# Performance work log

Measured on AMD Instinct MI355X. Metric: run time of the kernel, lower is better.

Reference implementation:

```python
import jax, jax.numpy as jnp
import numpy as np

B, H, W, D, C = 1, 32, 32, 32, 256
WS = (8, 8, 8)
SS = (4, 4, 4)
NH = 8
HD = C // NH
N = WS[0] * WS[1] * WS[2]
NW = (H // WS[0]) * (W // WS[1]) * (D // WS[2])


def _rel_pos_index():
    coords = np.stack(np.meshgrid(np.arange(WS[0]), np.arange(WS[1]), np.arange(WS[2]), indexing='ij'))
    cf = coords.reshape(3, -1)
    rc = (cf[:, :, None] - cf[:, None, :]).transpose(1, 2, 0).astype(np.int64)
    rc[:, :, 0] += WS[0] - 1
    rc[:, :, 1] += WS[1] - 1
    rc[:, :, 2] += WS[2] - 1
    rc[:, :, 0] *= (2 * WS[2] - 1) * (2 * WS[1] - 1)
    rc[:, :, 1] *= (2 * WS[2] - 1)
    return rc.sum(-1).reshape(-1)  # [N*N]


def _attn_mask():
    m = np.zeros((H, W, D), np.float32)
    cnt = 0

    def sl(ws, ss):
        return ((0, -ws), (-ws, -ss), (-ss, None))

    for hs in sl(WS[0], SS[0]):
        for ws_ in sl(WS[1], SS[1]):
            for ds in sl(WS[2], SS[2]):
                m[hs[0]:hs[1], ws_[0]:ws_[1], ds[0]:ds[1]] = cnt
                cnt += 1
    m = m.reshape(H // WS[0], WS[0], W // WS[1], WS[1], D // WS[2], WS[2])
    m = m.transpose(0, 2, 4, 1, 3, 5).reshape(NW, N)
    diff = m[:, None, :] - m[:, :, None]  # [NW, N, N]
    return np.where(diff != 0, -100.0, 0.0).astype(np.float32)


REL_IDX = jnp.asarray(_rel_pos_index())
ATTN_MASK = jnp.asarray(_attn_mask())  # [NW, N, N]


def setup_inputs() -> dict:
    key = jax.random.key(0)
    ks = jax.random.split(key, 4)
    return {
        'x': jax.random.normal(ks[0], (B, H, W, D, C), jnp.float32),
        'qkv_weight': jax.random.normal(ks[1], (3 * C, C), jnp.float32) * 0.02,
        'qkv_bias': jnp.zeros((3 * C,), jnp.float32),
        'proj_weight': jax.random.normal(ks[2], (C, C), jnp.float32) * 0.02,
        'proj_bias': jnp.zeros((C,), jnp.float32),
        'rpb_table': jax.random.normal(ks[3], ((2 * WS[0] - 1) * (2 * WS[1] - 1) * (2 * WS[2] - 1), NH), jnp.float32) * 0.02,
    }


def reference(x, qkv_weight, qkv_bias, proj_weight, proj_bias, rpb_table):
    # cyclic shift
    xs = jnp.roll(x, (-SS[0], -SS[1], -SS[2]), axis=(1, 2, 3))
    # window partition -> [B*NW, N, C]
    xw = xs.reshape(B, H // WS[0], WS[0], W // WS[1], WS[1], D // WS[2], WS[2], C)
    xw = xw.transpose(0, 1, 3, 5, 2, 4, 6, 7).reshape(B * NW, N, C)
    # qkv projection
    qkv = xw @ qkv_weight.T + qkv_bias
    qkv = qkv.reshape(B * NW, N, 3, NH, HD).transpose(2, 0, 3, 1, 4)  # [3, B*NW, NH, N, HD]
    q, k, v = qkv[0] * (HD ** -0.5), qkv[1], qkv[2]
    # relative position bias [NH, N, N]
    bias = rpb_table[REL_IDX].reshape(N, N, NH).transpose(2, 0, 1)
    attn = jnp.einsum('whnd,whmd->whnm', q, k) + bias[None]
    # shift mask per window
    attn = attn.reshape(B, NW, NH, N, N) + ATTN_MASK[None, :, None]
    attn = jax.nn.softmax(attn.reshape(B * NW, NH, N, N), axis=-1)
    out = jnp.einsum('whnm,whmd->whnd', attn, v)
    out = out.transpose(0, 2, 1, 3).reshape(B * NW, N, C)
    out = out @ proj_weight.T + proj_bias
    # un-window -> [B, H, W, D, C]
    out = out.reshape(B, H // WS[0], W // WS[1], D // WS[2], WS[0], WS[1], WS[2], C)
    out = out.transpose(0, 1, 4, 2, 5, 3, 6, 7).reshape(B, H, W, D, C)
    # reverse cyclic shift
    return jnp.roll(out, (SS[0], SS[1], SS[2]), axis=(1, 2, 3))
```

## Files before the change

### kernel.cpp

```cpp
#include <hip/hip_runtime.h>

typedef __attribute__((ext_vector_type(8))) short short8;
typedef __attribute__((ext_vector_type(4))) short s4v;
typedef __attribute__((ext_vector_type(2))) uint uint2v;
typedef __attribute__((ext_vector_type(4))) float floatx4;

#define CCH   256
#define QSCALE 0.17677669529663687f
#define LOG2E  1.4426950408889634f

__device__ __forceinline__ unsigned short f2bf(float f) {
    unsigned u = __float_as_uint(f);
    u = u + 0x7fffu + ((u >> 16) & 1u);
    return (unsigned short)(u >> 16);
}

__device__ __forceinline__ uint pk2bf(float a, float b) {
    uint ua = __float_as_uint(a) + 0x8000u;
    uint ub = __float_as_uint(b) + 0x8000u;
    return __builtin_amdgcn_perm(ub, ua, 0x07060302u);
}

__device__ __forceinline__ void gl_lds16(const void* g, void* l) {
    __builtin_amdgcn_global_load_lds((const __attribute__((address_space(1))) void*)g,
                                     (__attribute__((address_space(3))) void*)l, 16, 0, 0);
}

__device__ __forceinline__ int spatial_off(int token) {
    int w = token >> 9, n = token & 511;
    int wh = w >> 4, ww = (w >> 2) & 3, wd = w & 3;
    int h1 = n >> 6, w1 = (n >> 3) & 7, d1 = n & 7;
    int gh = (wh * 8 + h1 + 4) & 31;
    int gw = (ww * 8 + w1 + 4) & 31;
    int gd = (wd * 8 + d1 + 4) & 31;
    return ((gh * 32 + gw) * 32 + gd) * CCH;
}

__global__ __launch_bounds__(256) void xconv(const float* __restrict__ x,
                                             ushort* __restrict__ Xw) {
    int tid = blockIdx.x * 256 + threadIdx.x;
    int token = tid >> 5, c8 = (tid & 31) * 8;
    const float* src = x + spatial_off(token) + c8;
    float4 a = *(const float4*)src;
    float4 b = *(const float4*)(src + 4);
    uint2v lo, hi;
    lo[0] = pk2bf(a.x, a.y);
    lo[1] = pk2bf(a.z, a.w);
    hi[0] = pk2bf(b.x, b.y);
    hi[1] = pk2bf(b.z, b.w);
    uint2v* dst = (uint2v*)(Xw + (size_t)token * 256 + c8);
    dst[0] = lo;
    dst[1] = hi;
}

__global__ __launch_bounds__(256) void wconv(const float* __restrict__ Wq,
                                             const float* __restrict__ Wp,
                                             ushort* __restrict__ Wqb,
                                             ushort* __restrict__ Wpb) {
    int tid = blockIdx.x * 256 + threadIdx.x;
    if (tid < 196608) {
        float s = (tid < 65536) ? (QSCALE * LOG2E) : 1.0f;
        Wqb[tid] = f2bf(Wq[tid] * s);
    } else {
        int i = tid - 196608;
        Wpb[i] = f2bf(Wp[i]);
    }
}

__global__ __launch_bounds__(256) void pair_prep(const float* __restrict__ rpb,
                                                 uint* __restrict__ Up) {
    int tid = blockIdx.x * 256 + threadIdx.x;
    if (tid >= 27000) return;
    int head = tid / 3375, idx = tid - head * 3375;
    uint lo = f2bf(rpb[idx * 8 + head] * LOG2E);
    uint hi = f2bf(rpb[(idx > 0 ? idx - 1 : 0) * 8 + head] * LOG2E);
    Up[tid] = lo | (hi << 16);
}

__global__ __launch_bounds__(256) void gemm_qkv(
    const ushort* __restrict__ A,
    const ushort* __restrict__ Bw,
    const float* __restrict__ bq,
    ushort* __restrict__ Q, ushort* __restrict__ K, ushort* __restrict__ Vf) {
    __shared__ short As[128 * 64];
    __shared__ short Bs[128 * 64];
    const int t = threadIdx.x;
    const int wv = t >> 6, lane = t & 63, quad = lane >> 4, col = lane & 15;
    const int m0 = blockIdx.y * 128, n0 = blockIdx.x * 128;
    const int wm = (wv & 1) * 64, wn = (wv >> 1) * 64;

    floatx4 zf = {0.f, 0.f, 0.f, 0.f};
    floatx4 acc[4][4];
#pragma unroll
    for (int i = 0; i < 4; ++i)
#pragma unroll
        for (int j = 0; j < 4; ++j) acc[i][j] = zf;

    for (int kk = 0; kk < 256; kk += 64) {
        __syncthreads();
#pragma unroll
        for (int i = 0; i < 4; ++i) {
            int s = i * 256 + t;
            int row = s >> 3, qs = s & 7;
            int qg = qs ^ (row & 7);
            gl_lds16(A + (size_t)(m0 + row) * 256 + kk + qg * 8,
                     As + (i * 256 + wv * 64) * 8);
        }
#pragma unroll
        for (int i = 0; i < 4; ++i) {
            int s = i * 256 + t;
            int row = s >> 3, qs = s & 7;
            int qg = qs ^ (row & 7);
            gl_lds16(Bw + (size_t)(n0 + row) * 256 + kk + qg * 8,
                     Bs + (i * 256 + wv * 64) * 8);
        }
        __syncthreads();
#pragma unroll
        for (int h = 0; h < 2; ++h) {
            short8 af[4], bf[4];
#pragma unroll
            for (int mi = 0; mi < 4; ++mi) {
                int row = wm + mi * 16 + col;
                af[mi] = *(const short8*)(As + (row * 8 + ((h * 4 + quad) ^ (row & 7))) * 8);
            }
#pragma unroll
            for (int ni = 0; ni < 4; ++ni) {
                int row = wn + ni * 16 + col;
                bf[ni] = *(const short8*)(Bs + (row * 8 + ((h * 4 + quad) ^ (row & 7))) * 8);
            }
#pragma unroll
            for (int mi = 0; mi < 4; ++mi)
#pragma unroll
                for (int ni = 0; ni < 4; ++ni)
                    acc[mi][ni] = __builtin_amdgcn_mfma_f32_16x16x32_bf16(af[mi], bf[ni], acc[mi][ni], 0, 0, 0);
        }
    }

#pragma unroll
    for (int ni = 0; ni < 4; ++ni) {
        int j = n0 + wn + ni * 16 + col;
        int three = j >> 8, head = (j >> 5) & 7, hd = j & 31;
        float bias = bq[j] * ((j < 256) ? (QSCALE * LOG2E) : 1.0f);
        if (three == 2) {
            int h = hd >> 4, colv = hd & 15;
#pragma unroll
            for (int mi = 0; mi < 4; ++mi) {
                int mb = m0 + wm + mi * 16 + quad * 4;
                int w = mb >> 9, n = mb & 511;
                size_t off = ((size_t)((w * 8 + head) * 64 + (n >> 4) * 2 + h) << 8)
                           + ((((n >> 2) & 3) * 16 + colv) << 2);
                uint2v pv;
                pv[0] = pk2bf(acc[mi][ni][0] + bias, acc[mi][ni][1] + bias);
                pv[1] = pk2bf(acc[mi][ni][2] + bias, acc[mi][ni][3] + bias);
                *(uint2v*)(Vf + off) = pv;
            }
        } else {
            ushort* dst = (three == 0) ? Q : K;
#pragma unroll
            for (int mi = 0; mi < 4; ++mi) {
#pragma unroll
                for (int r = 0; r < 4; ++r) {
                    int m = m0 + wm + mi * 16 + quad * 4 + r;
                    int w = m >> 9, n = m & 511;
                    dst[((size_t)(w * 8 + head) * 512 + n) * 32 + hd] = f2bf(acc[mi][ni][r] + bias);
                }
            }
        }
    }
}

__global__ __launch_bounds__(256) void gemm_proj(
    const ushort* __restrict__ A,
    const ushort* __restrict__ Bw,
    const float* __restrict__ bp,
    float* __restrict__ out) {
    __shared__ short As[128 * 64];
    __shared__ short Bs[128 * 64];
    const int t = threadIdx.x;
    const int wv = t >> 6, lane = t & 63, quad = lane >> 4, col = lane & 15;
    const int m0 = blockIdx.y * 128, n0 = blockIdx.x * 128;
    const int wm = (wv & 1) * 64, wn = (wv >> 1) * 64;

    floatx4 zf = {0.f, 0.f, 0.f, 0.f};
    floatx4 acc[4][4];
#pragma unroll
    for (int i = 0; i < 4; ++i)
#pragma unroll
        for (int j = 0; j < 4; ++j) acc[i][j] = zf;

    for (int kk = 0; kk < 256; kk += 64) {
        __syncthreads();
#pragma unroll
        for (int i = 0; i < 4; ++i) {
            int s = i * 256 + t;
            int row = s >> 3, qs = s & 7;
            int qg = qs ^ (row & 7);
            gl_lds16(A + (size_t)(m0 + row) * 256 + kk + qg * 8,
                     As + (i * 256 + wv * 64) * 8);
        }
#pragma unroll
        for (int i = 0; i < 4; ++i) {
            int s = i * 256 + t;
            int row = s >> 3, qs = s & 7;
            int qg = qs ^ (row & 7);
            gl_lds16(Bw + (size_t)(n0 + row) * 256 + kk + qg * 8,
                     Bs + (i * 256 + wv * 64) * 8);
        }
        __syncthreads();
#pragma unroll
        for (int h = 0; h < 2; ++h) {
            short8 af[4], bf[4];
#pragma unroll
            for (int mi = 0; mi < 4; ++mi) {
                int row = wm + mi * 16 + col;
                af[mi] = *(const short8*)(As + (row * 8 + ((h * 4 + quad) ^ (row & 7))) * 8);
            }
#pragma unroll
            for (int ni = 0; ni < 4; ++ni) {
                int row = wn + ni * 16 + col;
                bf[ni] = *(const short8*)(Bs + (row * 8 + ((h * 4 + quad) ^ (row & 7))) * 8);
            }
#pragma unroll
            for (int mi = 0; mi < 4; ++mi)
#pragma unroll
                for (int ni = 0; ni < 4; ++ni)
                    acc[mi][ni] = __builtin_amdgcn_mfma_f32_16x16x32_bf16(af[mi], bf[ni], acc[mi][ni], 0, 0, 0);
        }
    }

#pragma unroll
    for (int ni = 0; ni < 4; ++ni) {
        int j = n0 + wn + ni * 16 + col;
        float bias = bp[j];
#pragma unroll
        for (int mi = 0; mi < 4; ++mi) {
#pragma unroll
            for (int r = 0; r < 4; ++r) {
                int m = m0 + wm + mi * 16 + quad * 4 + r;
                out[spatial_off(m) + j] = acc[mi][ni][r] + bias;
            }
        }
    }
}

__global__ __launch_bounds__(256, 2) void attn_kernel(
    const ushort* __restrict__ Q, const ushort* __restrict__ K,
    const ushort* __restrict__ Vf, const uint* __restrict__ Up,
    ushort* __restrict__ Y) {
    __shared__ short Kl[512 * 32];
    __shared__ short Vs[64 * 256];
    __shared__ uint  Ul[3375];

    const int t = threadIdx.x;
    const int bid = blockIdx.x;
    const int w = bid >> 3, head = bid & 7;
    const int wh = w >> 4, ww = (w >> 2) & 3, wd = w & 3;
    const int wv = t >> 6, lane = t & 63, quad = lane >> 4, col = lane & 15;

    const ushort* Kg = K + (size_t)(w * 8 + head) * 512 * 32;
    const ushort* Vg = Vf + (size_t)(w * 8 + head) * 512 * 32;
    const ushort* Qg = Q + (size_t)(w * 8 + head) * 512 * 32;

#pragma unroll
    for (int i = 0; i < 8; ++i) {
        gl_lds16(Kg + (size_t)(i * 256 + t) * 8, Kl + (i * 256 + wv * 64) * 8);
        gl_lds16(Vg + (size_t)(i * 256 + t) * 8, Vs + (i * 256 + wv * 64) * 8);
    }
    const uint* Uph = Up + head * 3375;
    for (int i = t; i < 3375; i += 256) Ul[i] = Uph[i];
    __syncthreads();

    const bool boundary = (wh == 3) | (ww == 3) | (wd == 3);
    floatx4 zf = {0.f, 0.f, 0.f, 0.f};

    for (int qs = 0; qs < 8; ++qs) {
        const int qt = wv * 8 + qs;
        const short8 qf = *(const short8*)(Qg + (size_t)(qt * 16 + col) * 32 + quad * 8);

        const int qrow = qt * 16 + col;
        const int qh = qrow >> 6, qw = (qrow >> 3) & 7, qd = qrow & 7;
        const int Base0 = ((qh + 7) * 15 + (qw + 7 - (quad >> 1))) * 15
                        + (qd - ((quad & 1) << 2) + 7);
        const int cq = ((wh == 3) ? (1 + ((qrow >> 8) & 1)) * 16 : 0)
                     + ((ww == 3) ? (1 + ((qrow >> 5) & 1)) * 4 : 0)
                     + ((wd == 3) ? (1 + ((qrow >> 2) & 1)) : 0);

        float rs = 0.f;
        floatx4 o0 = zf, o1 = zf;

        for (int c = 0; c < 2; ++c) {
            const short* KlC = Kl + c * 8192;
            const short* VsC = Vs + c * 8192;
            const int BaseC = Base0 - c * 900;
            const int ckh = (wh == 3) ? ((1 + c) * 16) : 0;

            floatx4 acc[16];
#pragma unroll
            for (int tt = 0; tt < 16; ++tt) {
                const int Kt2 = ((tt >> 2) * 15 + (tt & 3) * 2) * 15;
                uint p0 = Ul[BaseC - Kt2];
                uint p1 = Ul[BaseC - Kt2 - 2];
                floatx4 cf;
                cf[0] = __uint_as_float(p0 << 16);
                cf[1] = __uint_as_float(p0 & 0xffff0000u);
                cf[2] = __uint_as_float(p1 << 16);
                cf[3] = __uint_as_float(p1 & 0xffff0000u);
                if (boundary) {
                    int ck = ckh
                           + ((ww == 3) ? (1 + ((tt >> 1) & 1)) * 4 : 0)
                           + ((wd == 3) ? (1 + (quad & 1)) : 0);
                    float madd = (cq == ck) ? 0.f : -144.269504f;
                    cf[0] += madd; cf[1] += madd; cf[2] += madd; cf[3] += madd;
                }
                short8 kf = *(const short8*)(KlC + tt * 512 + col * 32 + quad * 8);
                acc[tt] = __builtin_amdgcn_mfma_f32_16x16x32_bf16(kf, qf, cf, 0, 0, 0);
            }

#pragma unroll
            for (int tt = 0; tt < 16; ++tt) {
                float e0 = exp2f(acc[tt][0]);
                float e1 = exp2f(acc[tt][1]);
                float e2 = exp2f(acc[tt][2]);
                float e3 = exp2f(acc[tt][3]);
                rs += (e0 + e1) + (e2 + e3);
                uint2v pp;
                pp[0] = pk2bf(e0, e1);
                pp[1] = pk2bf(e2, e3);
                s4v pf = __builtin_bit_cast(s4v, pp);
                s4v v0 = *(const s4v*)(VsC + ((tt * 2 + 0) << 8) + lane * 4);
                s4v v1 = *(const s4v*)(VsC + ((tt * 2 + 1) << 8) + lane * 4);
                o0 = __builtin_amdgcn_mfma_f32_16x16x16bf16_1k(v0, pf, o0, 0, 0, 0);
                o1 = __builtin_amdgcn_mfma_f32_16x16x16bf16_1k(v1, pf, o1, 0, 0, 0);
            }
        }

        rs += __shfl_xor(rs, 16);
        rs += __shfl_xor(rs, 32);
        const float inv = __builtin_amdgcn_rcpf(rs);

        int token = w * 512 + qt * 16 + col;
        ushort* Yb = Y + (size_t)token * 256 + head * 32 + quad * 4;
        uint2v y0, y1;
        y0[0] = pk2bf(o0[0] * inv, o0[1] * inv);
        y0[1] = pk2bf(o0[2] * inv, o0[3] * inv);
        y1[0] = pk2bf(o1[0] * inv, o1[1] * inv);
        y1[1] = pk2bf(o1[2] * inv, o1[3] * inv);
        *(uint2v*)(Yb) = y0;
        *(uint2v*)(Yb + 16) = y1;
    }
}

extern "C" void kernel_launch(void* const* d_in, const int* in_sizes, int n_in,
                              void* d_out, int out_size, void* d_ws, size_t ws_size,
                              hipStream_t stream) {
    const float* x      = (const float*)d_in[0];
    const float* qkv_w  = (const float*)d_in[1];
    const float* qkv_b  = (const float*)d_in[2];
    const float* proj_w = (const float*)d_in[3];
    const float* proj_b = (const float*)d_in[4];
    const float* rpb    = (const float*)d_in[5];
    float* out = (float*)d_out;

    ushort* Xw  = (ushort*)d_ws;
    ushort* Q   = Xw + 8388608;
    ushort* K   = Q + 8388608;
    ushort* Vf  = K + 8388608;
    ushort* Y   = Vf + 8388608;
    uint*   Up  = (uint*)(Y + 8388608);
    ushort* Wqb = (ushort*)(Up + 27008);
    ushort* Wpb = Wqb + 196608;

    xconv<<<dim3(4096), dim3(256), 0, stream>>>(x, Xw);
    wconv<<<dim3(1024), dim3(256), 0, stream>>>(qkv_w, proj_w, Wqb, Wpb);
    pair_prep<<<dim3(106), dim3(256), 0, stream>>>(rpb, Up);
    gemm_qkv<<<dim3(6, 256), dim3(256), 0, stream>>>(Xw, Wqb, qkv_b, Q, K, Vf);
    attn_kernel<<<dim3(512), dim3(256), 0, stream>>>(Q, K, Vf, Up, Y);
    gemm_proj<<<dim3(2, 256), dim3(256), 0, stream>>>(Y, Wpb, proj_b, out);
}
```

Baseline: 204.2 us.

## Drop LDS staging of K/V in attention and split each window-head across two blocks

The attention kernel no longer copies K and V into shared memory. It reads them directly from global memory, so LDS use falls to just the bias table, and launch bounds are raised to allow 4 blocks per CU. Each window-head is now split across two blocks (1024 blocks in total). Each wave processes 4 query tiles at once, so every K/V fragment load is reused across those 4 tiles, and exp2f is replaced by the hardware exp2 builtin. In exchange, K/V reads now depend on global/L2 latency and are repeated by both half-blocks, and the bias table is reloaded per block while register pressure rises.

Result: slower. 475.6 us (+132.9%).

```diff
diff --git a/kernel.cpp b/kernel.cpp
--- a/kernel.cpp
+++ b/kernel.cpp
@@ -243,17 +243,15 @@
     }
 }
 
-__global__ __launch_bounds__(256, 2) void attn_kernel(
+__global__ __launch_bounds__(256, 4) void attn_kernel(
     const ushort* __restrict__ Q, const ushort* __restrict__ K,
     const ushort* __restrict__ Vf, const uint* __restrict__ Up,
     ushort* __restrict__ Y) {
-    __shared__ short Kl[512 * 32];
-    __shared__ short Vs[64 * 256];
-    __shared__ uint  Ul[3375];
+    __shared__ uint Ul[3375];
 
     const int t = threadIdx.x;
     const int bid = blockIdx.x;
-    const int w = bid >> 3, head = bid & 7;
+    const int w = bid >> 4, head = (bid >> 1) & 7, half = bid & 1;
     const int wh = w >> 4, ww = (w >> 2) & 3, wd = w & 3;
     const int wv = t >> 6, lane = t & 63, quad = lane >> 4, col = lane & 15;
 
@@ -261,11 +259,6 @@
     const ushort* Vg = Vf + (size_t)(w * 8 + head) * 512 * 32;
     const ushort* Qg = Q + (size_t)(w * 8 + head) * 512 * 32;
 
-#pragma unroll
-    for (int i = 0; i < 8; ++i) {
-        gl_lds16(Kg + (size_t)(i * 256 + t) * 8, Kl + (i * 256 + wv * 64) * 8);
-        gl_lds16(Vg + (size_t)(i * 256 + t) * 8, Vs + (i * 256 + wv * 64) * 8);
-    }
     const uint* Uph = Up + head * 3375;
     for (int i = t; i < 3375; i += 256) Ul[i] = Uph[i];
     __syncthreads();
@@ -273,78 +266,89 @@
     const bool boundary = (wh == 3) | (ww == 3) | (wd == 3);
     floatx4 zf = {0.f, 0.f, 0.f, 0.f};
 
-    for (int qs = 0; qs < 8; ++qs) {
-        const int qt = wv * 8 + qs;
-        const short8 qf = *(const short8*)(Qg + (size_t)(qt * 16 + col) * 32 + quad * 8);
-
+    short8 qf[4];
+    int Base0q[4], cqq[4];
+#pragma unroll
+    for (int qi = 0; qi < 4; ++qi) {
+        const int qt = half * 16 + wv * 4 + qi;
+        qf[qi] = *(const short8*)(Qg + (size_t)(qt * 16 + col) * 32 + quad * 8);
         const int qrow = qt * 16 + col;
         const int qh = qrow >> 6, qw = (qrow >> 3) & 7, qd = qrow & 7;
-        const int Base0 = ((qh + 7) * 15 + (qw + 7 - (quad >> 1))) * 15
-                        + (qd - ((quad & 1) << 2) + 7);
-        const int cq = ((wh == 3) ? (1 + ((qrow >> 8) & 1)) * 16 : 0)
-                     + ((ww == 3) ? (1 + ((qrow >> 5) & 1)) * 4 : 0)
-                     + ((wd == 3) ? (1 + ((qrow >> 2) & 1)) : 0);
-
-        float rs = 0.f;
-        floatx4 o0 = zf, o1 = zf;
-
-        for (int c = 0; c < 2; ++c) {
-            const short* KlC = Kl + c * 8192;
-            const short* VsC = Vs + c * 8192;
-            const int BaseC = Base0 - c * 900;
-            const int ckh = (wh == 3) ? ((1 + c) * 16) : 0;
-
-            floatx4 acc[16];
-#pragma unroll
-            for (int tt = 0; tt < 16; ++tt) {
-                const int Kt2 = ((tt >> 2) * 15 + (tt & 3) * 2) * 15;
-                uint p0 = Ul[BaseC - Kt2];
-                uint p1 = Ul[BaseC - Kt2 - 2];
+        Base0q[qi] = ((qh + 7) * 15 + (qw + 7 - (quad >> 1))) * 15
+                   + (qd - ((quad & 1) << 2) + 7);
+        cqq[qi] = ((wh == 3) ? (1 + ((qrow >> 8) & 1)) * 16 : 0)
+                + ((ww == 3) ? (1 + ((qrow >> 5) & 1)) * 4 : 0)
+                + ((wd == 3) ? (1 + ((qrow >> 2) & 1)) : 0);
+    }
+
+    floatx4 o0[4], o1[4];
+    float rs[4] = {0.f, 0.f, 0.f, 0.f};
+#pragma unroll
+    for (int qi = 0; qi < 4; ++qi) { o0[qi] = zf; o1[qi] = zf; }
+
+#pragma unroll
+    for (int c = 0; c < 2; ++c) {
+        const int ckh = (wh == 3) ? ((1 + c) * 16) : 0;
+#pragma unroll
+        for (int tt = 0; tt < 16; ++tt) {
+            short8 kf = *(const short8*)(Kg + (size_t)((c * 256 + tt * 16 + col) * 32 + quad * 8));
+            s4v v0 = *(const s4v*)(Vg + ((c * 32 + tt * 2 + 0) << 8) + lane * 4);
+            s4v v1 = *(const s4v*)(Vg + ((c * 32 + tt * 2 + 1) << 8) + lane * 4);
+
+            const int Kt2 = ((tt >> 2) * 15 + (tt & 3) * 2) * 15 + c * 900;
+            int ckb = 0;
+            if (boundary)
+                ckb = ckh + ((ww == 3) ? (1 + ((tt >> 1) & 1)) * 4 : 0)
+                          + ((wd == 3) ? (1 + (quad & 1)) : 0);
+
+            floatx4 accq[4];
+#pragma unroll
+            for (int qi = 0; qi < 4; ++qi) {
+                uint p0 = Ul[Base0q[qi] - Kt2];
+                uint p1 = Ul[Base0q[qi] - Kt2 - 2];
                 floatx4 cf;
                 cf[0] = __uint_as_float(p0 << 16);
                 cf[1] = __uint_as_float(p0 & 0xffff0000u);
                 cf[2] = __uint_as_float(p1 << 16);
                 cf[3] = __uint_as_float(p1 & 0xffff0000u);
                 if (boundary) {
-                    int ck = ckh
-                           + ((ww == 3) ? (1 + ((tt >> 1) & 1)) * 4 : 0)
-                           + ((wd == 3) ? (1 + (quad & 1)) : 0);
-                    float madd = (cq == ck) ? 0.f : -144.269504f;
+                    float madd = (cqq[qi] == ckb) ? 0.f : -144.269504f;
                     cf[0] += madd; cf[1] += madd; cf[2] += madd; cf[3] += madd;
                 }
-                short8 kf = *(const short8*)(KlC + tt * 512 + col * 32 + quad * 8);
-                acc[tt] = __builtin_amdgcn_mfma_f32_16x16x32_bf16(kf, qf, cf, 0, 0, 0);
-            }
-
-#pragma unroll
-            for (int tt = 0; tt < 16; ++tt) {
-                float e0 = exp2f(acc[tt][0]);
-                float e1 = exp2f(acc[tt][1]);
-                float e2 = exp2f(acc[tt][2]);
-                float e3 = exp2f(acc[tt][3]);
-                rs += (e0 + e1) + (e2 + e3);
+                accq[qi] = __builtin_amdgcn_mfma_f32_16x16x32_bf16(kf, qf[qi], cf, 0, 0, 0);
+            }
+
+#pragma unroll
+            for (int qi = 0; qi < 4; ++qi) {
+                float e0 = __builtin_amdgcn_exp2f(accq[qi][0]);
+                float e1 = __builtin_amdgcn_exp2f(accq[qi][1]);
+                float e2 = __builtin_amdgcn_exp2f(accq[qi][2]);
+                float e3 = __builtin_amdgcn_exp2f(accq[qi][3]);
+                rs[qi] += (e0 + e1) + (e2 + e3);
                 uint2v pp;
                 pp[0] = pk2bf(e0, e1);
                 pp[1] = pk2bf(e2, e3);
                 s4v pf = __builtin_bit_cast(s4v, pp);
-                s4v v0 = *(const s4v*)(VsC + ((tt * 2 + 0) << 8) + lane * 4);
-                s4v v1 = *(const s4v*)(VsC + ((tt * 2 + 1) << 8) + lane * 4);
-                o0 = __builtin_amdgcn_mfma_f32_16x16x16bf16_1k(v0, pf, o0, 0, 0, 0);
-                o1 = __builtin_amdgcn_mfma_f32_16x16x16bf16_1k(v1, pf, o1, 0, 0, 0);
-            }
-        }
-
-        rs += __shfl_xor(rs, 16);
-        rs += __shfl_xor(rs, 32);
-        const float inv = __builtin_amdgcn_rcpf(rs);
-
+                o0[qi] = __builtin_amdgcn_mfma_f32_16x16x16bf16_1k(v0, pf, o0[qi], 0, 0, 0);
+                o1[qi] = __builtin_amdgcn_mfma_f32_16x16x16bf16_1k(v1, pf, o1[qi], 0, 0, 0);
+            }
+        }
+    }
+
+#pragma unroll
+    for (int qi = 0; qi < 4; ++qi) {
+        float r = rs[qi];
+        r += __shfl_xor(r, 16);
+        r += __shfl_xor(r, 32);
+        const float inv = __builtin_amdgcn_rcpf(r);
+        const int qt = half * 16 + wv * 4 + qi;
         int token = w * 512 + qt * 16 + col;
         ushort* Yb = Y + (size_t)token * 256 + head * 32 + quad * 4;
         uint2v y0, y1;
-        y0[0] = pk2bf(o0[0] * inv, o0[1] * inv);
-        y0[1] = pk2bf(o0[2] * inv, o0[3] * inv);
-        y1[0] = pk2bf(o1[0] * inv, o1[1] * inv);
-        y1[1] = pk2bf(o1[2] * inv, o1[3] * inv);
+        y0[0] = pk2bf(o0[qi][0] * inv, o0[qi][1] * inv);
+        y0[1] = pk2bf(o0[qi][2] * inv, o0[qi][3] * inv);
+        y1[0] = pk2bf(o1[qi][0] * inv, o1[qi][1] * inv);
+        y1[1] = pk2bf(o1[qi][2] * inv, o1[qi][3] * inv);
         *(uint2v*)(Yb) = y0;
         *(uint2v*)(Yb + 16) = y1;
     }
@@ -374,6 +378,6 @@
     wconv<<<dim3(1024), dim3(256), 0, stream>>>(qkv_w, proj_w, Wqb, Wpb);
     pair_prep<<<dim3(106), dim3(256), 0, stream>>>(rpb, Up);
     gemm_qkv<<<dim3(6, 256), dim3(256), 0, stream>>>(Xw, Wqb, qkv_b, Q, K, Vf);
-    attn_kernel<<<dim3(512), dim3(256), 0, stream>>>(Q, K, Vf, Up, Y);
+    attn_kernel<<<dim3(1024), dim3(256), 0, stream>>>(Q, K, Vf, Up, Y);
     gemm_proj<<<dim3(2, 256), dim3(256), 0, stream>>>(Y, Wpb, proj_b, out);
 }
```
